# Kernel tuning notes

Measured on AMD Instinct MI355X. Metric: run time of the kernel, lower is better.

The kernel has to match this reference:

```python
import jax, jax.numpy as jnp
import numpy as np

DRN = 0.4
TWO_PI = 2.0 * np.pi


def _mlp(x, ws, bs):
    # torch_geometric MLP with act='LeakyRelu' (slope 0.01), dropout=0 (eval), norm treated as identity (eval running stats)
    for w, b in zip(ws[:-1], bs[:-1]):
        x = jax.nn.leaky_relu(x @ w + b, 0.01)
    return x @ ws[-1] + bs[-1]


def _conv(x, ws, bs):
    # x: [B, N, F] = [pt, h..., ang_re, ang_im]. Dense masked equivalent of radius-graph EdgeConv.
    ang = x[..., -2:]
    d2 = jnp.sum((ang[:, :, None, :] - ang[:, None, :, :]) ** 2, -1)
    adj = (d2 <= DRN * DRN).astype(x.dtype)  # [B,N,N], i=target, j=source, self-loops included (radius ball)
    h = x[..., 1:-2]
    B, N, H = h.shape
    hi = jnp.broadcast_to(h[:, :, None, :], (B, N, N, H))
    hj = jnp.broadcast_to(h[:, None, :, :], (B, N, N, H))
    re, im = ang[..., 0], ang[..., 1]
    r2 = re * re + im * im
    nrm = jnp.maximum(jnp.sqrt(r2[:, :, None] * r2[:, None, :]), 1e-12)
    cos = (re[:, :, None] * re[:, None, :] + im[:, :, None] * im[:, None, :]) / nrm
    sin = (im[:, :, None] * re[:, None, :] - re[:, :, None] * im[:, None, :]) / nrm
    feat = jnp.concatenate([hi, hj, hj - hi, cos[..., None], sin[..., None]], -1)
    m = _mlp(feat, ws, bs)  # [B,N,N,H_out+1]
    # pt-weighted aggregation: message pt is the TARGET's pt (x_i[:, :1] in torch code)
    pt = x[..., 0]
    msg_pt = pt[:, :, None] * adj
    denom = jnp.sum(msg_pt, -1, keepdims=True)
    w = jnp.where(denom > 0, msg_pt / denom, 0.0)  # nan_to_num equivalent
    agg = jnp.einsum('bij,bijk->bik', w, m)
    sw = jnp.sum(w, -1)
    agg_pt = pt * sw                      # sum_j w * pt_i
    agg_ang = ang * sw[..., None]          # sum_j w * ang_i
    # phase renormalization: exp(2*pi*i*gamma) * (re + i*im)
    gamma = agg[..., -1]
    c, s = jnp.cos(TWO_PI * gamma), jnp.sin(TWO_PI * gamma)
    re2 = c * agg_ang[..., 0] - s * agg_ang[..., 1]
    im2 = s * agg_ang[..., 0] + c * agg_ang[..., 1]
    return jnp.concatenate([agg_pt[..., None], agg[..., :-1], re2[..., None], im2[..., None]], -1)


def _forward(pt, angles, c0w, c0b, c1w, c1b, rw, rb):
    absz = jnp.sqrt(jnp.sum(angles ** 2, -1))  # |view_as_complex(angles)|
    x = jnp.concatenate([pt[..., None], absz[..., None], angles], -1)
    x = _conv(x, c0w, c0b)
    x = _conv(x, c1w, c1b)
    # pt-weighted readout over particles
    ptf = x[..., 0]
    denom = jnp.sum(ptf, -1, keepdims=True)
    wj = jnp.where(denom > 0, ptf / denom, 0.0)
    xg = jnp.einsum('bn,bnf->bf', wj, x[..., 1:])
    logits = _mlp(xg[:, :-2], rw, rb)
    return jnp.concatenate([jax.nn.sigmoid(logits), xg[:, -2:]], -1)


def setup_inputs() -> dict:
    key = jax.random.key(0)
    ks = jax.random.split(key, 16)
    B, N = 128, 128
    pt = jax.random.uniform(ks[0], (B, N), jnp.float32, 0.05, 1.0)  # all > 0 so mask is all-true
    angles = 0.25 * jax.random.normal(ks[1], (B, N, 2), jnp.float32)

    def lin(k, i, o):
        return (0.2 / np.sqrt(i)) * jax.random.normal(k, (i, o), jnp.float32) * np.sqrt(i)

    H = 16
    return {
        'pt': pt, 'angles': angles,
        'c0_w0': lin(ks[2], 5, H), 'c0_b0': jnp.zeros((H,), jnp.float32),
        'c0_w1': lin(ks[3], H, H + 1), 'c0_b1': jnp.zeros((H + 1,), jnp.float32),
        'c1_w0': lin(ks[4], 3 * H + 2, H), 'c1_b0': jnp.zeros((H,), jnp.float32),
        'c1_w1': lin(ks[5], H, H + 1), 'c1_b1': jnp.zeros((H + 1,), jnp.float32),
        'r_w0': lin(ks[6], H, 32), 'r_b0': jnp.zeros((32,), jnp.float32),
        'r_w1': lin(ks[7], 32, 32), 'r_b1': jnp.zeros((32,), jnp.float32),
        'r_w2': lin(ks[8], 32, 1), 'r_b2': jnp.zeros((1,), jnp.float32),
    }


def reference(pt, angles, c0_w0, c0_b0, c0_w1, c0_b1, c1_w0, c1_b0, c1_w1, c1_b1, r_w0, r_b0, r_w1, r_b1, r_w2, r_b2):
    return _forward(pt, angles, (c0_w0, c0_w1), (c0_b0, c0_b1), (c1_w0, c1_w1), (c1_b0, c1_b1), (r_w0, r_w1, r_w2), (r_b0, r_b1, r_b2))
```

## Files before the change

kernel.cpp:

```cpp
#include <hip/hip_runtime.h>
#include <math.h>


#define BB 128
#define NN 128
#define BN (BB * NN)

typedef float f32x2 __attribute__((ext_vector_type(2)));

__device__ __forceinline__ f32x2 pk2(float s) { f32x2 r; r[0] = s; r[1] = s; return r; }
__device__ __forceinline__ f32x2 pkfma(f32x2 a, f32x2 b, f32x2 c) {
    return __builtin_elementwise_fma(a, b, c);
}
__device__ __forceinline__ f32x2 pkmax(f32x2 a, f32x2 b) {
    return __builtin_elementwise_max(a, b);
}

template <int CTRL>
__device__ __forceinline__ float dpp_add(float x) {
    int tmp = __builtin_amdgcn_update_dpp(0, __float_as_int(x), CTRL, 0xF, 0xF, true);
    return x + __int_as_float(tmp);
}

__device__ __forceinline__ float grp16_sum(float x) {
    x = dpp_add<0xB1>(x);
    x = dpp_add<0x4E>(x);
    x = dpp_add<0x114>(x);
    x = dpp_add<0x118>(x);
    return x;
}

__device__ __forceinline__ float bcast_grp(float x, int bidx) {
    return __int_as_float(__builtin_amdgcn_ds_bpermute(bidx, __float_as_int(x)));
}

__global__ __launch_bounds__(256) void conv0_kernel(
    const float* __restrict__ ang,
    const float* __restrict__ w0,
    const float* __restrict__ b0,
    const float* __restrict__ w1,
    const float* __restrict__ b1,
    const float* __restrict__ nw0,
    const float* __restrict__ nb0,
    float* __restrict__ ang1,
    float* __restrict__ u1,
    float* __restrict__ v1)
{
    const int tid  = threadIdx.x;
    const int lane = tid & 63;
    const int wid  = tid >> 6;
    const int t    = lane & 15;
    const int g    = lane >> 4;
    const int ni   = blockIdx.x * 16 + wid * 4 + g;
    const int base = (blockIdx.x >> 3) << 7;

    __shared__ float hls[16][17];

    const float2 ai = ((const float2*)ang)[ni];
    const float r2i = fmaf(ai.x, ai.x, ai.y * ai.y);
    const float abszi = __builtin_amdgcn_sqrtf(r2i);
    const float invi  = __builtin_amdgcn_rsqf(r2i);

    f32x2 u0b2[8], q02[8], wc2[8], ws2[8];
    #pragma unroll
    for (int p = 0; p < 8; ++p) {
        f32x2 wa  = *(const f32x2*)(w0 + 2 * p);
        f32x2 wb  = *(const f32x2*)(w0 + 16 + 2 * p);
        f32x2 wcv = *(const f32x2*)(w0 + 32 + 2 * p);
        f32x2 bb  = *(const f32x2*)(b0 + 2 * p);
        u0b2[p] = pkfma(pk2(abszi), wa - wcv, bb);
        q02[p]  = wb + wcv;
        wc2[p]  = *(const f32x2*)(w0 + 48 + 2 * p);
        ws2[p]  = *(const f32x2*)(w0 + 64 + 2 * p);
    }

    float w1row[16], w1g[16];
    #pragma unroll
    for (int k = 0; k < 16; ++k) {
        w1row[k] = w1[k * 17 + t];
        w1g[k]   = w1[k * 17 + 16];
    }
    const float b1t = b1[t], b1g = b1[16];

    const int o   = lane & 31;
    const int kk  = o & 15;
    const bool isU = (o < 16);
    float wk[16];
    {
        const int off = isU ? 0 : 256;
        #pragma unroll
        for (int c = 0; c < 16; ++c) {
            float a_ = nw0[off + c * 16 + kk];
            float c_ = nw0[512 + c * 16 + kk];
            wk[c] = isU ? (a_ - c_) : (a_ + c_);
        }
    }
    const float accb = isU ? nb0[kk] : 0.0f;

    f32x2 A2[8];
    #pragma unroll
    for (int p = 0; p < 8; ++p) A2[p] = pk2(0.0f);
    float degf = 0.0f;

    #pragma unroll 4
    for (int jj = 0; jj < 8; ++jj) {
        const float2 aj = ((const float2*)ang)[base + jj * 16 + t];
        const float r2j = fmaf(aj.x, aj.x, aj.y * aj.y);
        const float abszj = __builtin_amdgcn_sqrtf(r2j);
        const float ivj   = __builtin_amdgcn_rsqf(r2j);
        const float dre = ai.x - aj.x, dim = ai.y - aj.y;
        const float d2 = fmaf(dre, dre, dim * dim);
        const float adjf = (d2 <= 0.16f) ? 1.0f : 0.0f;
        degf += adjf;
        const float inv = fminf(invi * ivj, 1e12f);
        const f32x2 cos2 = pk2(fmaf(ai.x, aj.x, ai.y * aj.y) * inv);
        const f32x2 sin2 = pk2(fmaf(ai.y, aj.x, -(ai.x * aj.y)) * inv);
        const f32x2 ab2 = pk2(abszj);
        const f32x2 adj2 = pk2(adjf);
        #pragma unroll
        for (int p = 0; p < 8; ++p) {
            f32x2 z = pkfma(ab2, q02[p], u0b2[p]);
            z = pkfma(cos2, wc2[p], z);
            z = pkfma(sin2, ws2[p], z);
            f32x2 a = pkmax(z, z * 0.01f);
            A2[p] = pkfma(a, adj2, A2[p]);
        }
    }

    const int bidx = (lane | 15) << 2;
    float Ak[16];
    #pragma unroll
    for (int p = 0; p < 8; ++p) {
        Ak[2 * p]     = bcast_grp(grp16_sum(A2[p][0]), bidx);
        Ak[2 * p + 1] = bcast_grp(grp16_sum(A2[p][1]), bidx);
    }
    const float degA = bcast_grp(grp16_sum(degf), bidx);
    const float invdeg = __builtin_amdgcn_rcpf(degA);

    float s = 0.0f, sg = 0.0f;
    #pragma unroll
    for (int k = 0; k < 16; ++k) {
        s  = fmaf(Ak[k], w1row[k], s);
        sg = fmaf(Ak[k], w1g[k], sg);
    }
    const float mt    = fmaf(s, invdeg, b1t);
    const float gamma = fmaf(sg, invdeg, b1g);

    {
        const float gf = gamma - floorf(gamma);
        const float cs = __builtin_amdgcn_cosf(gf);
        const float sn = __builtin_amdgcn_sinf(gf);
        const float re2 = cs * ai.x - sn * ai.y;
        const float im2 = fmaf(sn, ai.x, cs * ai.y);
        if (t == 0) ((float4*)ang1)[ni] = make_float4(re2, im2, invi, 0.0f);
    }

    hls[wid * 4 + g][t] = mt;

    #pragma unroll
    for (int p = 0; p < 2; ++p) {
        const int nl = (lane >> 5) + 2 * p;
        const int node = wid * 4 + nl;
        float acc = accb;
        #pragma unroll
        for (int c = 0; c < 16; ++c) acc = fmaf(hls[node][c], wk[c], acc);
        const int nout = (blockIdx.x * 16 + node);
        if (isU) u1[nout * 16 + kk] = acc;
        else     v1[nout * 16 + kk] = acc;
    }
}

__global__ __launch_bounds__(256) void conv1_kernel(
    const float* __restrict__ pt,
    const float* __restrict__ ang1,
    const float* __restrict__ u1,
    const float* __restrict__ v1,
    const float* __restrict__ w0,
    const float* __restrict__ w1,
    const float* __restrict__ b1,
    float* __restrict__ part)
{
    const int tid  = threadIdx.x;
    const int lane = tid & 63;
    const int wid  = tid >> 6;
    const int t    = lane & 15;
    const int g    = lane >> 4;
    const int ni   = blockIdx.x * 16 + wid * 4 + g;
    const int base = (blockIdx.x >> 3) << 7;

    const float4 a4 = ((const float4*)ang1)[ni];
    const float rei = a4.x, imi = a4.y, invi = a4.z;
    const float ptf = pt[ni];

    f32x2 u0b2[8], wc2[8], ws2[8];
    {
        const float4* ug = (const float4*)(u1 + (size_t)ni * 16);
        float4 q0 = ug[0], q1 = ug[1], q2 = ug[2], q3 = ug[3];
        u0b2[0][0] = q0.x; u0b2[0][1] = q0.y; u0b2[1][0] = q0.z; u0b2[1][1] = q0.w;
        u0b2[2][0] = q1.x; u0b2[2][1] = q1.y; u0b2[3][0] = q1.z; u0b2[3][1] = q1.w;
        u0b2[4][0] = q2.x; u0b2[4][1] = q2.y; u0b2[5][0] = q2.z; u0b2[5][1] = q2.w;
        u0b2[6][0] = q3.x; u0b2[6][1] = q3.y; u0b2[7][0] = q3.z; u0b2[7][1] = q3.w;
    }
    #pragma unroll
    for (int p = 0; p < 8; ++p) {
        wc2[p] = *(const f32x2*)(w0 + 768 + 2 * p);
        ws2[p] = *(const f32x2*)(w0 + 784 + 2 * p);
    }

    float w1row[16], w1g[16];
    #pragma unroll
    for (int k = 0; k < 16; ++k) {
        w1row[k] = w1[k * 17 + t];
        w1g[k]   = w1[k * 17 + 16];
    }
    const float b1t = b1[t], b1g = b1[16];

    f32x2 A2[8];
    #pragma unroll
    for (int p = 0; p < 8; ++p) A2[p] = pk2(0.0f);
    float degf = 0.0f;

    #pragma unroll 4
    for (int jj = 0; jj < 8; ++jj) {
        const int j = base + jj * 16 + t;
        const float4 aj = ((const float4*)ang1)[j];
        f32x2 vj2[8];
        {
            const float4* vg = (const float4*)(v1 + (size_t)j * 16);
            float4 q0 = vg[0], q1 = vg[1], q2 = vg[2], q3 = vg[3];
            vj2[0][0] = q0.x; vj2[0][1] = q0.y; vj2[1][0] = q0.z; vj2[1][1] = q0.w;
            vj2[2][0] = q1.x; vj2[2][1] = q1.y; vj2[3][0] = q1.z; vj2[3][1] = q1.w;
            vj2[4][0] = q2.x; vj2[4][1] = q2.y; vj2[5][0] = q2.z; vj2[5][1] = q2.w;
            vj2[6][0] = q3.x; vj2[6][1] = q3.y; vj2[7][0] = q3.z; vj2[7][1] = q3.w;
        }
        const float dre = rei - aj.x, dim = imi - aj.y;
        const float d2 = fmaf(dre, dre, dim * dim);
        const float adjf = (d2 <= 0.16f) ? 1.0f : 0.0f;
        degf += adjf;
        const float inv = fminf(invi * aj.z, 1e12f);
        const f32x2 cos2 = pk2(fmaf(rei, aj.x, imi * aj.y) * inv);
        const f32x2 sin2 = pk2(fmaf(imi, aj.x, -(rei * aj.y)) * inv);
        const f32x2 adj2 = pk2(adjf);
        #pragma unroll
        for (int p = 0; p < 8; ++p) {
            f32x2 z = u0b2[p] + vj2[p];
            z = pkfma(cos2, wc2[p], z);
            z = pkfma(sin2, ws2[p], z);
            f32x2 a = pkmax(z, z * 0.01f);
            A2[p] = pkfma(a, adj2, A2[p]);
        }
    }

    const int bidx = (lane | 15) << 2;
    float Ak[16];
    #pragma unroll
    for (int p = 0; p < 8; ++p) {
        Ak[2 * p]     = bcast_grp(grp16_sum(A2[p][0]), bidx);
        Ak[2 * p + 1] = bcast_grp(grp16_sum(A2[p][1]), bidx);
    }
    const float degA = bcast_grp(grp16_sum(degf), bidx);
    const float invdeg = __builtin_amdgcn_rcpf(degA);

    float s = 0.0f, sg = 0.0f;
    #pragma unroll
    for (int k = 0; k < 16; ++k) {
        s  = fmaf(Ak[k], w1row[k], s);
        sg = fmaf(Ak[k], w1g[k], sg);
    }
    const float mt    = fmaf(s, invdeg, b1t);
    const float gamma = fmaf(sg, invdeg, b1g);

    const float gf = gamma - floorf(gamma);
    const float cs = __builtin_amdgcn_cosf(gf);
    const float sn = __builtin_amdgcn_sinf(gf);
    const float re2 = cs * rei - sn * imi;
    const float im2 = fmaf(sn, rei, cs * imi);

    float pm  = ptf * mt;
    float pre = ptf * re2;
    float pim = ptf * im2;
    float ppt = ptf;
    pm  += __int_as_float(__builtin_amdgcn_ds_swizzle(__float_as_int(pm),  0x401F));
    pre += __int_as_float(__builtin_amdgcn_ds_swizzle(__float_as_int(pre), 0x401F));
    pim += __int_as_float(__builtin_amdgcn_ds_swizzle(__float_as_int(pim), 0x401F));
    ppt += __int_as_float(__builtin_amdgcn_ds_swizzle(__float_as_int(ppt), 0x401F));
    pm  += __shfl_xor(pm, 32);
    pre += __shfl_xor(pre, 32);
    pim += __shfl_xor(pim, 32);
    ppt += __shfl_xor(ppt, 32);

    float* po = part + (size_t)(blockIdx.x * 4 + wid) * 20;
    if (lane < 16)       po[lane] = pm;
    else if (lane == 16) po[16] = pre;
    else if (lane == 17) po[17] = pim;
    else if (lane == 18) po[18] = ppt;
}

__global__ __launch_bounds__(64) void readout_kernel(
    const float* __restrict__ part,
    const float* __restrict__ w0, const float* __restrict__ b0,
    const float* __restrict__ w1, const float* __restrict__ b1,
    const float* __restrict__ w2, const float* __restrict__ b2,
    float* __restrict__ out) {
    const int b = blockIdx.x;
    const int t = threadIdx.x;

    __shared__ float sbuf[19];
    __shared__ float xg[18];
    __shared__ float h1r[32];

    if (t < 19) {
        float s0 = 0.0f, s1 = 0.0f, s2 = 0.0f, s3 = 0.0f;
        const float* pb = part + (size_t)b * 32 * 20 + t;
        #pragma unroll
        for (int r = 0; r < 32; r += 4) {
            s0 += pb[(r + 0) * 20];
            s1 += pb[(r + 1) * 20];
            s2 += pb[(r + 2) * 20];
            s3 += pb[(r + 3) * 20];
        }
        sbuf[t] = (s0 + s1) + (s2 + s3);
    }
    const float invd = __builtin_amdgcn_rcpf(sbuf[18]);
    if (t < 18) xg[t] = sbuf[t] * invd;

    if (t < 32) {
        float h = b0[t];
        #pragma unroll
        for (int k = 0; k < 16; ++k) h = fmaf(xg[k], w0[k * 32 + t], h);
        h = fmaxf(h, 0.01f * h);
        h1r[t] = h;
    }
    if (t < 32) {
        float h = b1[t];
        #pragma unroll
        for (int k = 0; k < 32; ++k) h = fmaf(h1r[k], w1[k * 32 + t], h);
        h = fmaxf(h, 0.01f * h);
        float p = h * w2[t];
        #pragma unroll
        for (int off = 16; off; off >>= 1) p += __shfl_xor(p, off);
        if (t == 0) {
            out[b * 3 + 0] = 1.0f / (1.0f + expf(-(p + b2[0])));
            out[b * 3 + 1] = xg[16];
            out[b * 3 + 2] = xg[17];
        }
    }
}

extern "C" void kernel_launch(void* const* d_in, const int* in_sizes, int n_in,
                              void* d_out, int out_size, void* d_ws, size_t ws_size,
                              hipStream_t stream) {
    const float* pt    = (const float*)d_in[0];
    const float* ang   = (const float*)d_in[1];
    const float* c0_w0 = (const float*)d_in[2];
    const float* c0_b0 = (const float*)d_in[3];
    const float* c0_w1 = (const float*)d_in[4];
    const float* c0_b1 = (const float*)d_in[5];
    const float* c1_w0 = (const float*)d_in[6];
    const float* c1_b0 = (const float*)d_in[7];
    const float* c1_w1 = (const float*)d_in[8];
    const float* c1_b1 = (const float*)d_in[9];
    const float* r_w0  = (const float*)d_in[10];
    const float* r_b0  = (const float*)d_in[11];
    const float* r_w1  = (const float*)d_in[12];
    const float* r_b1  = (const float*)d_in[13];
    const float* r_w2  = (const float*)d_in[14];
    const float* r_b2  = (const float*)d_in[15];
    float* out = (float*)d_out;
    float* ws = (float*)d_ws;

    float* ang1  = ws;
    float* u1    = ang1 + (size_t)BN * 4;
    float* v1    = u1 + (size_t)BN * 16;
    float* partb = v1 + (size_t)BN * 16;

    hipLaunchKernelGGL(conv0_kernel, dim3(BN / 16), dim3(256), 0, stream,
                       ang, c0_w0, c0_b0, c0_w1, c0_b1, c1_w0, c1_b0,
                       ang1, u1, v1);
    hipLaunchKernelGGL(conv1_kernel, dim3(BN / 16), dim3(256), 0, stream,
                       pt, ang1, u1, v1, c1_w0, c1_w1, c1_b1, partb);
    hipLaunchKernelGGL(readout_kernel, dim3(BB), dim3(64), 0, stream,
                       partb, r_w0, r_b0, r_w1, r_b1, r_w2, r_b2, out);
}
```

Before: 30.13 us.

## Split neighbor loop across two half-waves per node to double block count

Each target node is now handled by 32 lanes, with the source range split into two halves of 64, instead of 16 lanes over all 128 sources. Grids double in both conv kernels and the readout sums 64 partials per batch. The added half-wave sum uses a swizzle, and the second linear layer's weights are read inside the epilogue instead of being held in registers. The aim is more parallelism and latency hiding with lower register pressure, at the cost of extra reductions and redundant epilogue work per node.

```diff
diff --git a/kernel.cpp b/kernel.cpp
--- a/kernel.cpp
+++ b/kernel.cpp
@@ -30,8 +30,16 @@
     return x;
 }
 
-__device__ __forceinline__ float bcast_grp(float x, int bidx) {
+__device__ __forceinline__ float swz16_add(float x) {
+    return x + __int_as_float(__builtin_amdgcn_ds_swizzle(__float_as_int(x), 0x401F));
+}
+
+__device__ __forceinline__ float bcast31(float x, int bidx) {
     return __int_as_float(__builtin_amdgcn_ds_bpermute(bidx, __float_as_int(x)));
+}
+
+__device__ __forceinline__ float node_sum(float x, int bidx) {
+    return bcast31(swz16_add(grp16_sum(x)), bidx);
 }
 
 __global__ __launch_bounds__(256) void conv0_kernel(
@@ -51,10 +59,12 @@
     const int wid  = tid >> 6;
     const int t    = lane & 15;
     const int g    = lane >> 4;
-    const int ni   = blockIdx.x * 16 + wid * 4 + g;
-    const int base = (blockIdx.x >> 3) << 7;
-
-    __shared__ float hls[16][17];
+    const int nloc = g >> 1;
+    const int jh   = g & 1;
+    const int ni   = blockIdx.x * 8 + wid * 2 + nloc;
+    const int base = (blockIdx.x >> 4) << 7;
+
+    __shared__ float hls[8][17];
 
     const float2 ai = ((const float2*)ang)[ni];
     const float r2i = fmaf(ai.x, ai.x, ai.y * ai.y);
@@ -74,37 +84,14 @@
         ws2[p]  = *(const f32x2*)(w0 + 64 + 2 * p);
     }
 
-    float w1row[16], w1g[16];
-    #pragma unroll
-    for (int k = 0; k < 16; ++k) {
-        w1row[k] = w1[k * 17 + t];
-        w1g[k]   = w1[k * 17 + 16];
-    }
-    const float b1t = b1[t], b1g = b1[16];
-
-    const int o   = lane & 31;
-    const int kk  = o & 15;
-    const bool isU = (o < 16);
-    float wk[16];
-    {
-        const int off = isU ? 0 : 256;
-        #pragma unroll
-        for (int c = 0; c < 16; ++c) {
-            float a_ = nw0[off + c * 16 + kk];
-            float c_ = nw0[512 + c * 16 + kk];
-            wk[c] = isU ? (a_ - c_) : (a_ + c_);
-        }
-    }
-    const float accb = isU ? nb0[kk] : 0.0f;
-
     f32x2 A2[8];
     #pragma unroll
     for (int p = 0; p < 8; ++p) A2[p] = pk2(0.0f);
     float degf = 0.0f;
 
     #pragma unroll 4
-    for (int jj = 0; jj < 8; ++jj) {
-        const float2 aj = ((const float2*)ang)[base + jj * 16 + t];
+    for (int jj = 0; jj < 4; ++jj) {
+        const float2 aj = ((const float2*)ang)[base + jh * 64 + jj * 16 + t];
         const float r2j = fmaf(aj.x, aj.x, aj.y * aj.y);
         const float abszj = __builtin_amdgcn_sqrtf(r2j);
         const float ivj   = __builtin_amdgcn_rsqf(r2j);
@@ -127,24 +114,23 @@
         }
     }
 
-    const int bidx = (lane | 15) << 2;
+    const int bidx = (lane | 31) << 2;
     float Ak[16];
     #pragma unroll
     for (int p = 0; p < 8; ++p) {
-        Ak[2 * p]     = bcast_grp(grp16_sum(A2[p][0]), bidx);
-        Ak[2 * p + 1] = bcast_grp(grp16_sum(A2[p][1]), bidx);
-    }
-    const float degA = bcast_grp(grp16_sum(degf), bidx);
-    const float invdeg = __builtin_amdgcn_rcpf(degA);
+        Ak[2 * p]     = node_sum(A2[p][0], bidx);
+        Ak[2 * p + 1] = node_sum(A2[p][1], bidx);
+    }
+    const float invdeg = __builtin_amdgcn_rcpf(node_sum(degf, bidx));
 
     float s = 0.0f, sg = 0.0f;
     #pragma unroll
     for (int k = 0; k < 16; ++k) {
-        s  = fmaf(Ak[k], w1row[k], s);
-        sg = fmaf(Ak[k], w1g[k], sg);
-    }
-    const float mt    = fmaf(s, invdeg, b1t);
-    const float gamma = fmaf(sg, invdeg, b1g);
+        s  = fmaf(Ak[k], w1[k * 17 + t], s);
+        sg = fmaf(Ak[k], w1[k * 17 + 16], sg);
+    }
+    const float mt    = fmaf(s, invdeg, b1[t]);
+    const float gamma = fmaf(sg, invdeg, b1[16]);
 
     {
         const float gf = gamma - floorf(gamma);
@@ -152,22 +138,29 @@
         const float sn = __builtin_amdgcn_sinf(gf);
         const float re2 = cs * ai.x - sn * ai.y;
         const float im2 = fmaf(sn, ai.x, cs * ai.y);
-        if (t == 0) ((float4*)ang1)[ni] = make_float4(re2, im2, invi, 0.0f);
-    }
-
-    hls[wid * 4 + g][t] = mt;
-
-    #pragma unroll
-    for (int p = 0; p < 2; ++p) {
-        const int nl = (lane >> 5) + 2 * p;
-        const int node = wid * 4 + nl;
-        float acc = accb;
-        #pragma unroll
-        for (int c = 0; c < 16; ++c) acc = fmaf(hls[node][c], wk[c], acc);
-        const int nout = (blockIdx.x * 16 + node);
-        if (isU) u1[nout * 16 + kk] = acc;
-        else     v1[nout * 16 + kk] = acc;
-    }
+        if (jh == 0 && t == 0) ((float4*)ang1)[ni] = make_float4(re2, im2, invi, 0.0f);
+    }
+
+    hls[wid * 2 + nloc][t] = mt;
+
+    const int pn  = lane >> 5;
+    const int o   = lane & 31;
+    const int kk  = o & 15;
+    const bool isU = (o < 16);
+    float acc = isU ? nb0[kk] : 0.0f;
+    {
+        const int off = isU ? 0 : 256;
+        const float sgn = isU ? -1.0f : 1.0f;
+        #pragma unroll
+        for (int c = 0; c < 16; ++c) {
+            const float a_ = nw0[off + c * 16 + kk];
+            const float c_ = nw0[512 + c * 16 + kk];
+            acc = fmaf(hls[wid * 2 + pn][c], fmaf(sgn, c_, a_), acc);
+        }
+    }
+    const int nout = blockIdx.x * 8 + wid * 2 + pn;
+    if (isU) u1[nout * 16 + kk] = acc;
+    else     v1[nout * 16 + kk] = acc;
 }
 
 __global__ __launch_bounds__(256) void conv1_kernel(
@@ -185,8 +178,10 @@
     const int wid  = tid >> 6;
     const int t    = lane & 15;
     const int g    = lane >> 4;
-    const int ni   = blockIdx.x * 16 + wid * 4 + g;
-    const int base = (blockIdx.x >> 3) << 7;
+    const int nloc = g >> 1;
+    const int jh   = g & 1;
+    const int ni   = blockIdx.x * 8 + wid * 2 + nloc;
+    const int base = (blockIdx.x >> 4) << 7;
 
     const float4 a4 = ((const float4*)ang1)[ni];
     const float rei = a4.x, imi = a4.y, invi = a4.z;
@@ -207,22 +202,14 @@
         ws2[p] = *(const f32x2*)(w0 + 784 + 2 * p);
     }
 
-    float w1row[16], w1g[16];
-    #pragma unroll
-    for (int k = 0; k < 16; ++k) {
-        w1row[k] = w1[k * 17 + t];
-        w1g[k]   = w1[k * 17 + 16];
-    }
-    const float b1t = b1[t], b1g = b1[16];
-
     f32x2 A2[8];
     #pragma unroll
     for (int p = 0; p < 8; ++p) A2[p] = pk2(0.0f);
     float degf = 0.0f;
 
-    #pragma unroll 4
-    for (int jj = 0; jj < 8; ++jj) {
-        const int j = base + jj * 16 + t;
+    #pragma unroll 2
+    for (int jj = 0; jj < 4; ++jj) {
+        const int j = base + jh * 64 + jj * 16 + t;
         const float4 aj = ((const float4*)ang1)[j];
         f32x2 vj2[8];
         {
@@ -251,24 +238,23 @@
         }
     }
 
-    const int bidx = (lane | 15) << 2;
+    const int bidx = (lane | 31) << 2;
     float Ak[16];
     #pragma unroll
     for (int p = 0; p < 8; ++p) {
-        Ak[2 * p]     = bcast_grp(grp16_sum(A2[p][0]), bidx);
-        Ak[2 * p + 1] = bcast_grp(grp16_sum(A2[p][1]), bidx);
-    }
-    const float degA = bcast_grp(grp16_sum(degf), bidx);
-    const float invdeg = __builtin_amdgcn_rcpf(degA);
+        Ak[2 * p]     = node_sum(A2[p][0], bidx);
+        Ak[2 * p + 1] = node_sum(A2[p][1], bidx);
+    }
+    const float invdeg = __builtin_amdgcn_rcpf(node_sum(degf, bidx));
 
     float s = 0.0f, sg = 0.0f;
     #pragma unroll
     for (int k = 0; k < 16; ++k) {
-        s  = fmaf(Ak[k], w1row[k], s);
-        sg = fmaf(Ak[k], w1g[k], sg);
-    }
-    const float mt    = fmaf(s, invdeg, b1t);
-    const float gamma = fmaf(sg, invdeg, b1g);
+        s  = fmaf(Ak[k], w1[k * 17 + t], s);
+        sg = fmaf(Ak[k], w1[k * 17 + 16], sg);
+    }
+    const float mt    = fmaf(s, invdeg, b1[t]);
+    const float gamma = fmaf(sg, invdeg, b1[16]);
 
     const float gf = gamma - floorf(gamma);
     const float cs = __builtin_amdgcn_cosf(gf);
@@ -276,18 +262,15 @@
     const float re2 = cs * rei - sn * imi;
     const float im2 = fmaf(sn, rei, cs * imi);
 
-    float pm  = ptf * mt;
-    float pre = ptf * re2;
-    float pim = ptf * im2;
-    float ppt = ptf;
-    pm  += __int_as_float(__builtin_amdgcn_ds_swizzle(__float_as_int(pm),  0x401F));
-    pre += __int_as_float(__builtin_amdgcn_ds_swizzle(__float_as_int(pre), 0x401F));
-    pim += __int_as_float(__builtin_amdgcn_ds_swizzle(__float_as_int(pim), 0x401F));
-    ppt += __int_as_float(__builtin_amdgcn_ds_swizzle(__float_as_int(ppt), 0x401F));
-    pm  += __shfl_xor(pm, 32);
-    pre += __shfl_xor(pre, 32);
-    pim += __shfl_xor(pim, 32);
-    ppt += __shfl_xor(ppt, 32);
+    const float sel = (jh == 0) ? 1.0f : 0.0f;
+    float pm  = sel * ptf * mt;
+    float pre = sel * ptf * re2;
+    float pim = sel * ptf * im2;
+    float ppt = sel * ptf;
+    pm  = swz16_add(pm);   pm  += __shfl_xor(pm, 32);
+    pre = swz16_add(pre);  pre += __shfl_xor(pre, 32);
+    pim = swz16_add(pim);  pim += __shfl_xor(pim, 32);
+    ppt = swz16_add(ppt);  ppt += __shfl_xor(ppt, 32);
 
     float* po = part + (size_t)(blockIdx.x * 4 + wid) * 20;
     if (lane < 16)       po[lane] = pm;
@@ -311,9 +294,9 @@
 
     if (t < 19) {
         float s0 = 0.0f, s1 = 0.0f, s2 = 0.0f, s3 = 0.0f;
-        const float* pb = part + (size_t)b * 32 * 20 + t;
-        #pragma unroll
-        for (int r = 0; r < 32; r += 4) {
+        const float* pb = part + (size_t)b * 64 * 20 + t;
+        #pragma unroll
+        for (int r = 0; r < 64; r += 4) {
             s0 += pb[(r + 0) * 20];
             s1 += pb[(r + 1) * 20];
             s2 += pb[(r + 2) * 20];
@@ -374,10 +357,10 @@
     float* v1    = u1 + (size_t)BN * 16;
     float* partb = v1 + (size_t)BN * 16;
 
-    hipLaunchKernelGGL(conv0_kernel, dim3(BN / 16), dim3(256), 0, stream,
+    hipLaunchKernelGGL(conv0_kernel, dim3(BN / 8), dim3(256), 0, stream,
                        ang, c0_w0, c0_b0, c0_w1, c0_b1, c1_w0, c1_b0,
                        ang1, u1, v1);
-    hipLaunchKernelGGL(conv1_kernel, dim3(BN / 16), dim3(256), 0, stream,
+    hipLaunchKernelGGL(conv1_kernel, dim3(BN / 8), dim3(256), 0, stream,
                        pt, ang1, u1, v1, c1_w0, c1_w1, c1_b1, partb);
     hipLaunchKernelGGL(readout_kernel, dim3(BB), dim3(64), 0, stream,
                        partb, r_w0, r_b0, r_w1, r_b1, r_w2, r_b2, out);
```

New measurement: 31.14 us. 3.3% more time.
